# Kernel optimization log

Measured on AMD Instinct MI355X. Metric: run time of the kernel, lower is better.

Reference implementation:

```python
import jax, jax.numpy as jnp
import numpy as np

B, S, D, H, W = 8, 2048, 128, 8, 64
INT_HEADS = 8          # hardcoded in SpatioTemporalLayer1
EPS_COS = 1e-8
EPS_LN = 1e-5


def _mha(q_in, k_in, v_in, in_w, in_b, out_w, out_b, nh, mask=None):
    # q_in/k_in/v_in: (batch, len, d); torch nn.MultiheadAttention math (eval, no dropout)
    b, lq, d = q_in.shape
    hd = d // nh
    q = (q_in @ in_w[:d].T + in_b[:d]).reshape(b, lq, nh, hd)
    k = (k_in @ in_w[d:2 * d].T + in_b[d:2 * d]).reshape(b, k_in.shape[1], nh, hd)
    v = (v_in @ in_w[2 * d:].T + in_b[2 * d:]).reshape(b, v_in.shape[1], nh, hd)
    scores = jnp.einsum('bihd,bjhd->bhij', q, k) / jnp.sqrt(jnp.asarray(hd, q_in.dtype))
    if mask is not None:
        scores = scores + mask
    attn = jax.nn.softmax(scores, axis=-1)
    out = jnp.einsum('bhij,bjhd->bihd', attn, v).reshape(b, lq, d)
    return out @ out_w.T + out_b


def _layernorm(x, g, b):
    mu = x.mean(-1, keepdims=True)
    var = ((x - mu) ** 2).mean(-1, keepdims=True)
    return (x - mu) * jax.lax.rsqrt(var + EPS_LN) * g + b


def _cos_normalize(e):
    n = jnp.maximum(jnp.linalg.norm(e, axis=-1, keepdims=True), EPS_COS)
    return e / n


def _forward(x, spatial_info, temporal_info,
             lw_in_w, lw_in_b, lw_out_w, lw_out_b,
             spat_w, spat_b, temp_w, temp_b,
             int_in_w, int_in_b, int_out_w, int_out_b,
             ffn_w1, ffn_b1, ffn_w2, ffn_b2,
             ln1_g, ln1_b, ln2_g, ln2_b):
    b, s, d = x.shape
    # --- local window attention (S % W == 0 here, so no padding path) ---
    nw = s // W
    xw = x.reshape(b * nw, W, d)
    causal = jnp.triu(jnp.full((W, W), -jnp.inf, x.dtype), k=1)
    attn = _mha(xw, xw, xw, lw_in_w, lw_in_b, lw_out_w, lw_out_b, H, causal).reshape(b, s, d)
    x = _layernorm(attn + x, ln1_g, ln1_b)
    # --- FFN (torch nn.GELU default = exact erf) ---
    h = jax.nn.gelu(x @ ffn_w1.T + ffn_b1, approximate=False)
    x = _layernorm(h @ ffn_w2.T + ffn_b2 + x, ln2_g, ln2_b)
    # --- spatio-temporal interaction ---
    se = spatial_info @ spat_w.T + spat_b
    te = temporal_info @ temp_w.T + temp_b
    sn = _cos_normalize(se)
    tn = _cos_normalize(te)
    ss = jnp.einsum('bid,bjd->bij', sn, sn)   # (B,S,S) spatial cosine sim
    ts = jnp.einsum('bid,bjd->bij', tn, tn)   # (B,S,S) temporal cosine sim
    # interaction MHA is batch_first=False: it treats (B,S,D) as (len=B, batch=S, d).
    # Equivalent batch-first call on swapped axes (faithful to the torch source).
    inter = jnp.swapaxes(
        _mha(jnp.swapaxes(se, 0, 1), jnp.swapaxes(te, 0, 1), jnp.swapaxes(te, 0, 1),
             int_in_w, int_in_b, int_out_w, int_out_b, INT_HEADS), 0, 1)
    # similarity[b,i,j,d] = ss[b,i,j]*ts[b,i,j]*inter[b,i,d]; mean over j factorizes:
    sim = (ss * ts).mean(axis=2)              # (B,S)
    return x + sim[..., None] * inter


def setup_inputs() -> dict:
    key = jax.random.key(0)
    ks = jax.random.split(key, 24)
    sc = 0.02
    inp = {
        'x': jax.random.normal(ks[0], (B, S, D), jnp.float32),
        'spatial_info': jax.random.normal(ks[1], (B, S, D), jnp.float32),
        'temporal_info': jax.random.normal(ks[2], (B, S, D), jnp.float32),
        'lw_in_w': jax.random.normal(ks[3], (3 * D, D), jnp.float32) * sc,
        'lw_in_b': jnp.zeros((3 * D,), jnp.float32),
        'lw_out_w': jax.random.normal(ks[4], (D, D), jnp.float32) * sc,
        'lw_out_b': jnp.zeros((D,), jnp.float32),
        'spat_w': jax.random.normal(ks[5], (D, D), jnp.float32) * sc,
        'spat_b': jnp.zeros((D,), jnp.float32),
        'temp_w': jax.random.normal(ks[6], (D, D), jnp.float32) * sc,
        'temp_b': jnp.zeros((D,), jnp.float32),
        'int_in_w': jax.random.normal(ks[7], (3 * D, D), jnp.float32) * sc,
        'int_in_b': jnp.zeros((3 * D,), jnp.float32),
        'int_out_w': jax.random.normal(ks[8], (D, D), jnp.float32) * sc,
        'int_out_b': jnp.zeros((D,), jnp.float32),
        'ffn_w1': jax.random.normal(ks[9], (4 * D, D), jnp.float32) * sc,
        'ffn_b1': jnp.zeros((4 * D,), jnp.float32),
        'ffn_w2': jax.random.normal(ks[10], (D, 4 * D), jnp.float32) * sc,
        'ffn_b2': jnp.zeros((D,), jnp.float32),
        'ln1_g': jnp.ones((D,), jnp.float32),
        'ln1_b': jnp.zeros((D,), jnp.float32),
        'ln2_g': jnp.ones((D,), jnp.float32),
        'ln2_b': jnp.zeros((D,), jnp.float32),
    }
    return inp


def reference(x, spatial_info, temporal_info,
              lw_in_w, lw_in_b, lw_out_w, lw_out_b,
              spat_w, spat_b, temp_w, temp_b,
              int_in_w, int_in_b, int_out_w, int_out_b,
              ffn_w1, ffn_b1, ffn_w2, ffn_b2,
              ln1_g, ln1_b, ln2_g, ln2_b):
    return _forward(x, spatial_info, temporal_info,
                    lw_in_w, lw_in_b, lw_out_w, lw_out_b,
                    spat_w, spat_b, temp_w, temp_b,
                    int_in_w, int_in_b, int_out_w, int_out_b,
                    ffn_w1, ffn_b1, ffn_w2, ffn_b2,
                    ln1_g, ln1_b, ln2_g, ln2_b)
```

## Files before the change

kernel.cpp:

```cpp
#include <hip/hip_runtime.h>
#include <math.h>

#define BB 8
#define SS 2048
#define NTOK (BB * SS)

using bf16x8 = __attribute__((ext_vector_type(8))) short;
using f32x4  = __attribute__((ext_vector_type(4))) float;

__device__ __forceinline__ float gelu_tanh(float x) {
    float y = 0.7978845608f * (x + 0.044715f * x * x * x);
    float e = __expf(2.0f * y);
    float t = 1.0f - 2.0f / (e + 1.0f);
    return 0.5f * x * (1.0f + t);
}
__device__ __forceinline__ unsigned short f2b(float f) {
    unsigned int u = __float_as_uint(f);
    u += 0x7FFFu + ((u >> 16) & 1u);
    return (unsigned short)(u >> 16);
}
__device__ __forceinline__ float b2f(unsigned short u) {
    return __uint_as_float((unsigned int)u << 16);
}
__device__ __forceinline__ bf16x8 ldg_f32_b8(const float* p) {
    float4 f0 = *(const float4*)p, f1 = *(const float4*)(p + 4);
    union { ushort4 u[2]; bf16x8 v; } r;
    r.u[0] = (ushort4){f2b(f0.x), f2b(f0.y), f2b(f0.z), f2b(f0.w)};
    r.u[1] = (ushort4){f2b(f1.x), f2b(f1.y), f2b(f1.z), f2b(f1.w)};
    return r.v;
}

__global__ __launch_bounds__(256) void phase1(
    const float* __restrict__ x,
    const float* __restrict__ lw_in_w, const float* __restrict__ b_in,
    const float* __restrict__ lw_out_w, const float* __restrict__ b_out,
    const float* __restrict__ lng, const float* __restrict__ lnb,
    float* __restrict__ x1, unsigned short* __restrict__ x1b,
    const float* __restrict__ ffn_w1, const float* __restrict__ ffn_w2,
    unsigned short* __restrict__ Wb,
    const float* __restrict__ int_in_w, const float* __restrict__ int_out_w,
    unsigned short* __restrict__ Wib, unsigned short* __restrict__ Wiob,
    float* __restrict__ Mf,
    const float* __restrict__ spatial, const float* __restrict__ temporal,
    const float* __restrict__ spat_w, const float* __restrict__ temp_w,
    const float* __restrict__ bsp, const float* __restrict__ btp,
    unsigned short* __restrict__ snb, unsigned short* __restrict__ tnb,
    unsigned short* __restrict__ seb, unsigned short* __restrict__ teb)
{
    __shared__ unsigned short Qs[64 * 136];
    __shared__ unsigned short Ks[64 * 136];
    __shared__ unsigned short Vt[128 * 72];
    __shared__ unsigned short Pb[4][32 * 72];
    __shared__ float red[2][64][2];
    const int tid = threadIdx.x;
    const int wv = tid >> 6, lane = tid & 63, ln = lane & 15, q = lane >> 4;

    if (blockIdx.x >= 320) {
        const int idx2 = blockIdx.x - 320;
        const int y = idx2 >> 8;
        const int m0 = (idx2 & 255) * 64;
        const float* Af = y ? temporal : spatial;
        const float* Wf = y ? temp_w : spat_w;
        const float* bias = y ? btp : bsp;
        unsigned short* nb = y ? tnb : snb;
        unsigned short* raw = y ? teb : seb;
        const int wm = (wv >> 1) * 32, wn = (wv & 1) * 64;

        f32x4 acc[2][4] = {};
        #pragma unroll
        for (int kf = 0; kf < 4; ++kf) {
            bf16x8 a[2], b[4];
            #pragma unroll
            for (int fm = 0; fm < 2; ++fm)
                a[fm] = ldg_f32_b8(Af + (size_t)(m0 + wm + fm * 16 + ln) * 128 + kf * 32 + q * 8);
            #pragma unroll
            for (int fn = 0; fn < 4; ++fn)
                b[fn] = ldg_f32_b8(Wf + (size_t)(wn + fn * 16 + ln) * 128 + kf * 32 + q * 8);
            #pragma unroll
            for (int fm = 0; fm < 2; ++fm)
                #pragma unroll
                for (int fn = 0; fn < 4; ++fn)
                    acc[fm][fn] = __builtin_amdgcn_mfma_f32_16x16x32_bf16(a[fm], b[fn], acc[fm][fn], 0, 0, 0);
        }
        #pragma unroll
        for (int fm = 0; fm < 2; ++fm)
            #pragma unroll
            for (int r = 0; r < 4; ++r) {
                int rl = wm + fm * 16 + q * 4 + r;
                float s2 = 0.0f;
                #pragma unroll
                for (int fn = 0; fn < 4; ++fn) {
                    int col = wn + fn * 16 + ln;
                    float vv = acc[fm][fn][r] + bias[col];
                    acc[fm][fn][r] = vv;
                    s2 += vv * vv;
                }
                #pragma unroll
                for (int off = 1; off < 16; off <<= 1) s2 += __shfl_xor(s2, off, 64);
                if (ln == 0) red[0][rl][wv & 1] = s2;
            }
        __syncthreads();
        #pragma unroll
        for (int fm = 0; fm < 2; ++fm)
            #pragma unroll
            for (int r = 0; r < 4; ++r) {
                int rl = wm + fm * 16 + q * 4 + r;
                int row = m0 + rl;
                float inv = 1.0f / fmaxf(sqrtf(red[0][rl][0] + red[0][rl][1]), 1e-8f);
                #pragma unroll
                for (int fn = 0; fn < 4; ++fn) {
                    int col = wn + fn * 16 + ln;
                    float vv = acc[fm][fn][r];
                    nb[(size_t)row * 128 + col] = f2b(vv * inv);
                    raw[(size_t)row * 128 + col] = f2b(vv);
                }
            }
        return;
    }

    if (blockIdx.x >= 256) {
        int gt = (blockIdx.x - 256) * 256 + tid;
        #pragma unroll
        for (int s = 0; s < 3; ++s) {
            int v = gt + s * 16384;
            const float* src;
            unsigned short* dst;
            int off;
            if (v < 16384)      { src = ffn_w1;   dst = Wb;         off = v; }
            else if (v < 32768) { src = ffn_w2;   dst = Wb + 65536; off = v - 16384; }
            else if (v < 45056) { src = int_in_w; dst = Wib;        off = v - 32768; }
            else                { src = int_out_w; dst = Wiob;      off = v - 45056; }
            float4 f = *(const float4*)(src + (size_t)off * 4);
            *(ushort4*)(dst + (size_t)off * 4) =
                (ushort4){f2b(f.x), f2b(f.y), f2b(f.z), f2b(f.w)};
        }
        float4 z4 = (float4){0.f, 0.f, 0.f, 0.f};
        *(float4*)(Mf + (size_t)gt * 4) = z4;
        *(float4*)(Mf + (size_t)(gt + 16384) * 4) = z4;
        return;
    }

    const int m0 = blockIdx.x * 64;
    const int wm = (wv >> 1) * 32, wn = (wv & 1) * 64;

    bf16x8 afr[4][2];
    #pragma unroll
    for (int kf = 0; kf < 4; ++kf)
        #pragma unroll
        for (int fm = 0; fm < 2; ++fm)
            afr[kf][fm] = ldg_f32_b8(x + (size_t)(m0 + wm + fm * 16 + ln) * 128 + kf * 32 + q * 8);

    #pragma unroll
    for (int p = 0; p < 3; ++p) {
        f32x4 acc[2][4] = {};
        #pragma unroll
        for (int kf = 0; kf < 4; ++kf) {
            bf16x8 b[4];
            #pragma unroll
            for (int fn = 0; fn < 4; ++fn)
                b[fn] = ldg_f32_b8(lw_in_w + (size_t)(p * 128 + wn + fn * 16 + ln) * 128 + kf * 32 + q * 8);
            #pragma unroll
            for (int fm = 0; fm < 2; ++fm)
                #pragma unroll
                for (int fn = 0; fn < 4; ++fn)
                    acc[fm][fn] = __builtin_amdgcn_mfma_f32_16x16x32_bf16(afr[kf][fm], b[fn], acc[fm][fn], 0, 0, 0);
        }
        #pragma unroll
        for (int fm = 0; fm < 2; ++fm)
            #pragma unroll
            for (int r = 0; r < 4; ++r) {
                int rl = wm + fm * 16 + q * 4 + r;
                #pragma unroll
                for (int fn = 0; fn < 4; ++fn) {
                    int col = wn + fn * 16 + ln;
                    unsigned short v = f2b(acc[fm][fn][r] + b_in[p * 128 + col]);
                    if (p == 0)      Qs[rl * 136 + col] = v;
                    else if (p == 1) Ks[rl * 136 + col] = v;
                    else             Vt[col * 72 + rl] = v;
                }
            }
    }
    __syncthreads();

    {
        const int mh = wv >> 1, hq = wv & 1;
        unsigned short* P = &Pb[wv][0];
        #pragma unroll
        for (int hh = 0; hh < 4; ++hh) {
            const int h = hq * 4 + hh;
            f32x4 sacc[2][4] = {};
            bf16x8 az[2] = {}, bz[4] = {};
            if (q < 2) {
                #pragma unroll
                for (int fm = 0; fm < 2; ++fm)
                    az[fm] = *(const bf16x8*)&Qs[(mh * 32 + fm * 16 + ln) * 136 + h * 16 + q * 8];
                #pragma unroll
                for (int fn = 0; fn < 4; ++fn)
                    bz[fn] = *(const bf16x8*)&Ks[(fn * 16 + ln) * 136 + h * 16 + q * 8];
            }
            #pragma unroll
            for (int fm = 0; fm < 2; ++fm)
                #pragma unroll
                for (int fn = 0; fn < 4; ++fn)
                    sacc[fm][fn] = __builtin_amdgcn_mfma_f32_16x16x32_bf16(az[fm], bz[fn], sacc[fm][fn], 0, 0, 0);
            float invr[2][4];
            #pragma unroll
            for (int fm = 0; fm < 2; ++fm)
                #pragma unroll
                for (int r = 0; r < 4; ++r) {
                    int gi = mh * 32 + fm * 16 + q * 4 + r;
                    float mx = -1e30f;
                    #pragma unroll
                    for (int fn = 0; fn < 4; ++fn) {
                        int j = fn * 16 + ln;
                        float s = sacc[fm][fn][r] * 0.25f;
                        if (j > gi) s = -1e30f;
                        sacc[fm][fn][r] = s;
                        mx = fmaxf(mx, s);
                    }
                    #pragma unroll
                    for (int off = 1; off < 16; off <<= 1)
                        mx = fmaxf(mx, __shfl_xor(mx, off, 64));
                    float sum = 0.0f;
                    #pragma unroll
                    for (int fn = 0; fn < 4; ++fn) {
                        float p_ = __expf(sacc[fm][fn][r] - mx);
                        sacc[fm][fn][r] = p_;
                        sum += p_;
                    }
                    #pragma unroll
                    for (int off = 1; off < 16; off <<= 1)
                        sum += __shfl_xor(sum, off, 64);
                    invr[fm][r] = 1.0f / sum;
                    #pragma unroll
                    for (int fn = 0; fn < 4; ++fn)
                        P[(fm * 16 + q * 4 + r) * 72 + fn * 16 + ln] = f2b(sacc[fm][fn][r]);
                }
            f32x4 oacc[2] = {};
            #pragma unroll
            for (int kf2 = 0; kf2 < 2; ++kf2) {
                bf16x8 pa[2], vb;
                #pragma unroll
                for (int fm = 0; fm < 2; ++fm)
                    pa[fm] = *(const bf16x8*)&P[(fm * 16 + ln) * 72 + kf2 * 32 + q * 8];
                vb = *(const bf16x8*)&Vt[(h * 16 + ln) * 72 + kf2 * 32 + q * 8];
                #pragma unroll
                for (int fm = 0; fm < 2; ++fm)
                    oacc[fm] = __builtin_amdgcn_mfma_f32_16x16x32_bf16(pa[fm], vb, oacc[fm], 0, 0, 0);
            }
            #pragma unroll
            for (int fm = 0; fm < 2; ++fm)
                #pragma unroll
                for (int r = 0; r < 4; ++r)
                    Qs[(mh * 32 + fm * 16 + q * 4 + r) * 136 + h * 16 + ln] =
                        f2b(oacc[fm][r] * invr[fm][r]);
        }
    }
    __syncthreads();

    f32x4 acc[2][4] = {};
    #pragma unroll
    for (int kf = 0; kf < 4; ++kf) {
        bf16x8 a[2], b[4];
        #pragma unroll
        for (int fm = 0; fm < 2; ++fm)
            a[fm] = *(const bf16x8*)&Qs[(wm + fm * 16 + ln) * 136 + kf * 32 + q * 8];
        #pragma unroll
        for (int fn = 0; fn < 4; ++fn)
            b[fn] = ldg_f32_b8(lw_out_w + (size_t)(wn + fn * 16 + ln) * 128 + kf * 32 + q * 8);
        #pragma unroll
        for (int fm = 0; fm < 2; ++fm)
            #pragma unroll
            for (int fn = 0; fn < 4; ++fn)
                acc[fm][fn] = __builtin_amdgcn_mfma_f32_16x16x32_bf16(a[fm], b[fn], acc[fm][fn], 0, 0, 0);
    }
    #pragma unroll
    for (int fm = 0; fm < 2; ++fm)
        #pragma unroll
        for (int r = 0; r < 4; ++r) {
            int rl = wm + fm * 16 + q * 4 + r;
            int row = m0 + rl;
            float s1 = 0.0f, s2 = 0.0f;
            #pragma unroll
            for (int fn = 0; fn < 4; ++fn) {
                int col = wn + fn * 16 + ln;
                float vv = acc[fm][fn][r] + b_out[col] + x[(size_t)row * 128 + col];
                acc[fm][fn][r] = vv;
                s1 += vv; s2 += vv * vv;
            }
            #pragma unroll
            for (int off = 1; off < 16; off <<= 1) {
                s1 += __shfl_xor(s1, off, 64);
                s2 += __shfl_xor(s2, off, 64);
            }
            if (ln == 0) { red[0][rl][wv & 1] = s1; red[1][rl][wv & 1] = s2; }
        }
    __syncthreads();
    #pragma unroll
    for (int fm = 0; fm < 2; ++fm)
        #pragma unroll
        for (int r = 0; r < 4; ++r) {
            int rl = wm + fm * 16 + q * 4 + r;
            int row = m0 + rl;
            float mu = (red[0][rl][0] + red[0][rl][1]) * (1.0f / 128.0f);
            float var = (red[1][rl][0] + red[1][rl][1]) * (1.0f / 128.0f) - mu * mu;
            float rs = rsqrtf(var + 1e-5f);
            #pragma unroll
            for (int fn = 0; fn < 4; ++fn) {
                int col = wn + fn * 16 + ln;
                float o = (acc[fm][fn][r] - mu) * rs * lng[col] + lnb[col];
                x1[(size_t)row * 128 + col] = o;
                x1b[(size_t)row * 128 + col] = f2b(o);
            }
        }
}

__global__ __launch_bounds__(256) void phase2(
    const unsigned short* __restrict__ x1b, const float* __restrict__ x1,
    const unsigned short* __restrict__ Wb,
    const float* __restrict__ b1, const float* __restrict__ b2,
    const float* __restrict__ lng, const float* __restrict__ lnb,
    float* __restrict__ x2,
    const unsigned short* __restrict__ snb, const unsigned short* __restrict__ tnb,
    float* __restrict__ Mf)
{
    __shared__ __align__(16) char pool[36864];
    __shared__ float red[2][64][2];
    const int tid = threadIdx.x;
    const int wv = tid >> 6, lane = tid & 63, ln = lane & 15, q = lane >> 4;

    if (blockIdx.x < 256) {
        unsigned short* Xs = (unsigned short*)pool;
        unsigned short* Hs0 = (unsigned short*)(pool + 17408);
        unsigned short* Hs1 = (unsigned short*)(pool + 26624);
        const int t0 = blockIdx.x * 64;
        const int wm = (wv >> 1) * 32;
        const int wn1 = (wv & 1) * 32, wn2 = (wv & 1) * 64;
        const unsigned short* w1 = Wb;
        const unsigned short* w2 = Wb + 65536;

        const uint4* X4 = (const uint4*)(x1b + (size_t)t0 * 128);
        #pragma unroll
        for (int t = 0; t < 4; ++t) {
            int idx = tid + t * 256;
            int r = idx >> 4, c = idx & 15;
            *(uint4*)&Xs[r * 136 + c * 8] = X4[r * 16 + c];
        }
        __syncthreads();

        f32x4 acc2[2][4] = {};
        for (int ch = 0; ch < 8; ++ch) {
            const int hc0 = ch * 64;
            unsigned short* Hb = (ch & 1) ? Hs1 : Hs0;
            f32x4 acc1[2][2] = {};
            #pragma unroll
            for (int kf = 0; kf < 4; ++kf) {
                bf16x8 a[2], b[2];
                #pragma unroll
                for (int fm = 0; fm < 2; ++fm)
                    a[fm] = *(const bf16x8*)&Xs[(wm + fm * 16 + ln) * 136 + kf * 32 + q * 8];
                #pragma unroll
                for (int fn = 0; fn < 2; ++fn)
                    b[fn] = *(const bf16x8*)&w1[(size_t)(hc0 + wn1 + fn * 16 + ln) * 128 + kf * 32 + q * 8];
                #pragma unroll
                for (int fm = 0; fm < 2; ++fm)
                    #pragma unroll
                    for (int fn = 0; fn < 2; ++fn)
                        acc1[fm][fn] = __builtin_amdgcn_mfma_f32_16x16x32_bf16(a[fm], b[fn], acc1[fm][fn], 0, 0, 0);
            }
            #pragma unroll
            for (int fm = 0; fm < 2; ++fm)
                #pragma unroll
                for (int fn = 0; fn < 2; ++fn)
                    #pragma unroll
                    for (int r = 0; r < 4; ++r) {
                        int rl = wm + fm * 16 + q * 4 + r;
                        int col = wn1 + fn * 16 + ln;
                        Hb[rl * 72 + col] = f2b(gelu_tanh(acc1[fm][fn][r] + b1[hc0 + col]));
                    }
            __syncthreads();
            #pragma unroll
            for (int kf2 = 0; kf2 < 2; ++kf2) {
                bf16x8 a[2], b[4];
                #pragma unroll
                for (int fm = 0; fm < 2; ++fm)
                    a[fm] = *(const bf16x8*)&Hb[(wm + fm * 16 + ln) * 72 + kf2 * 32 + q * 8];
                #pragma unroll
                for (int fn = 0; fn < 4; ++fn)
                    b[fn] = *(const bf16x8*)&w2[(size_t)(wn2 + fn * 16 + ln) * 512 + hc0 + kf2 * 32 + q * 8];
                #pragma unroll
                for (int fm = 0; fm < 2; ++fm)
                    #pragma unroll
                    for (int fn = 0; fn < 4; ++fn)
                        acc2[fm][fn] = __builtin_amdgcn_mfma_f32_16x16x32_bf16(a[fm], b[fn], acc2[fm][fn], 0, 0, 0);
            }
        }
        #pragma unroll
        for (int fm = 0; fm < 2; ++fm)
            #pragma unroll
            for (int r = 0; r < 4; ++r) {
                int rl = wm + fm * 16 + q * 4 + r;
                int row = t0 + rl;
                float s1 = 0.0f, s2 = 0.0f;
                #pragma unroll
                for (int fn = 0; fn < 4; ++fn) {
                    int col = wn2 + fn * 16 + ln;
                    float vv = acc2[fm][fn][r] + b2[col] + x1[(size_t)row * 128 + col];
                    acc2[fm][fn][r] = vv;
                    s1 += vv; s2 += vv * vv;
                }
                #pragma unroll
                for (int off = 1; off < 16; off <<= 1) {
                    s1 += __shfl_xor(s1, off, 64);
                    s2 += __shfl_xor(s2, off, 64);
                }
                if (ln == 0) { red[0][rl][wv & 1] = s1; red[1][rl][wv & 1] = s2; }
            }
        __syncthreads();
        #pragma unroll
        for (int fm = 0; fm < 2; ++fm)
            #pragma unroll
            for (int r = 0; r < 4; ++r) {
                int rl = wm + fm * 16 + q * 4 + r;
                int row = t0 + rl;
                float mu = (red[0][rl][0] + red[0][rl][1]) * (1.0f / 128.0f);
                float var = (red[1][rl][0] + red[1][rl][1]) * (1.0f / 128.0f) - mu * mu;
                float rs = rsqrtf(var + 1e-5f);
                #pragma unroll
                for (int fn = 0; fn < 4; ++fn) {
                    int col = wn2 + fn * 16 + ln;
                    x2[(size_t)row * 128 + col] = (acc2[fm][fn][r] - mu) * rs * lng[col] + lnb[col];
                }
            }
        return;
    }

    {
        unsigned short* Sst = (unsigned short*)pool;
        unsigned short* Tst = (unsigned short*)(pool + 17408);
        const int idx2 = blockIdx.x - 256;
        const int d0 = (idx2 & 1) * 64, e0 = ((idx2 >> 1) & 1) * 64;
        const int z = idx2 >> 2;
        const int b = z >> 4, chunk = z & 15;
        const size_t rowb = (size_t)(b * SS + chunk * 128);

        #pragma unroll
        for (int it = 0; it < 4; ++it) {
            int j = (tid & 31) + it * 32;
            int c8 = (tid >> 5) * 8;
            uint4 sv = *(const uint4*)&snb[(rowb + j) * 128 + d0 + c8];
            uint4 tv = *(const uint4*)&tnb[(rowb + j) * 128 + e0 + c8];
            const unsigned short* sp = (const unsigned short*)&sv;
            const unsigned short* tp = (const unsigned short*)&tv;
            #pragma unroll
            for (int c = 0; c < 8; ++c) {
                Sst[(c8 + c) * 136 + j] = sp[c];
                Tst[(c8 + c) * 136 + j] = tp[c];
            }
        }
        __syncthreads();

        const int wm = (wv >> 1) * 32, wn = (wv & 1) * 32;
        f32x4 acc[2][2] = {};
        #pragma unroll
        for (int kf = 0; kf < 4; ++kf) {
            bf16x8 a[2], bb[2];
            #pragma unroll
            for (int fm = 0; fm < 2; ++fm)
                a[fm] = *(const bf16x8*)&Tst[(wm + fm * 16 + ln) * 136 + kf * 32 + q * 8];
            #pragma unroll
            for (int fn = 0; fn < 2; ++fn)
                bb[fn] = *(const bf16x8*)&Sst[(wn + fn * 16 + ln) * 136 + kf * 32 + q * 8];
            #pragma unroll
            for (int fm = 0; fm < 2; ++fm)
                #pragma unroll
                for (int fn = 0; fn < 2; ++fn)
                    acc[fm][fn] = __builtin_amdgcn_mfma_f32_16x16x32_bf16(a[fm], bb[fn], acc[fm][fn], 0, 0, 0);
        }
        float* pp = Mf + (size_t)b * 16384;
        #pragma unroll
        for (int fm = 0; fm < 2; ++fm)
            #pragma unroll
            for (int r = 0; r < 4; ++r) {
                int ee = e0 + wm + fm * 16 + q * 4 + r;
                #pragma unroll
                for (int fn = 0; fn < 2; ++fn) {
                    int dd = d0 + wn + fn * 16 + ln;
                    unsafeAtomicAdd(&pp[(size_t)ee * 128 + dd], acc[fm][fn][r]);
                }
            }
    }
}

__global__ __launch_bounds__(256) void simgemm_kernel(
    const unsigned short* __restrict__ snb, const unsigned short* __restrict__ tnb,
    const float* __restrict__ Mf, float* __restrict__ sim)
{
    __shared__ float red[64][2];
    const int tid = threadIdx.x, m0 = blockIdx.x * 64, b = m0 >> 11;
    const int wv = tid >> 6, lane = tid & 63, ln = lane & 15, q = lane >> 4;
    const int wm = (wv >> 1) * 32, wn = (wv & 1) * 64;

    f32x4 acc[2][4] = {};
    #pragma unroll
    for (int kf = 0; kf < 4; ++kf) {
        bf16x8 a[2], bb[4];
        #pragma unroll
        for (int fm = 0; fm < 2; ++fm)
            a[fm] = *(const bf16x8*)&snb[(size_t)(m0 + wm + fm * 16 + ln) * 128 + kf * 32 + q * 8];
        #pragma unroll
        for (int fn = 0; fn < 4; ++fn)
            bb[fn] = ldg_f32_b8(Mf + (size_t)b * 16384 + (size_t)(wn + fn * 16 + ln) * 128 + kf * 32 + q * 8);
        #pragma unroll
        for (int fm = 0; fm < 2; ++fm)
            #pragma unroll
            for (int fn = 0; fn < 4; ++fn)
                acc[fm][fn] = __builtin_amdgcn_mfma_f32_16x16x32_bf16(a[fm], bb[fn], acc[fm][fn], 0, 0, 0);
    }
    #pragma unroll
    for (int fm = 0; fm < 2; ++fm)
        #pragma unroll
        for (int r = 0; r < 4; ++r) {
            int rl = wm + fm * 16 + q * 4 + r;
            int row = m0 + rl;
            float s = 0.0f;
            #pragma unroll
            for (int fn = 0; fn < 4; ++fn) {
                int col = wn + fn * 16 + ln;
                s += acc[fm][fn][r] * b2f(tnb[(size_t)row * 128 + col]);
            }
            #pragma unroll
            for (int off = 1; off < 16; off <<= 1) s += __shfl_xor(s, off, 64);
            if (ln == 0) red[rl][wv & 1] = s;
        }
    __syncthreads();
    if (tid < 64) sim[m0 + tid] = (red[tid][0] + red[tid][1]) * (1.0f / (float)SS);
}

__global__ __launch_bounds__(256) void inter_block(
    const unsigned short* __restrict__ seb, const unsigned short* __restrict__ teb,
    const unsigned short* __restrict__ Wib,
    const float* __restrict__ b_int,
    const unsigned short* __restrict__ Wiob,
    const float* __restrict__ b_io,
    const float* __restrict__ sim, const float* __restrict__ x2,
    float* __restrict__ out)
{
    __shared__ unsigned short Qs[64 * 136];
    __shared__ unsigned short KVs[64 * 256];
    const int tid = threadIdx.x, s0 = blockIdx.x * 8;
    const int wv = tid >> 6, lane = tid & 63, ln = lane & 15, q = lane >> 4;
    const int wm = (wv >> 1) * 32, wn = (wv & 1) * 64;

    bf16x8 afr[4][2];
    #pragma unroll
    for (int kf = 0; kf < 4; ++kf)
        #pragma unroll
        for (int fm = 0; fm < 2; ++fm) {
            int rl = wm + fm * 16 + ln;
            size_t g = (size_t)(rl >> 3) * 2048 + s0 + (rl & 7);
            afr[kf][fm] = *(const bf16x8*)&seb[g * 128 + kf * 32 + q * 8];
        }

    #pragma unroll
    for (int p = 0; p < 3; ++p) {
        if (p == 1) {
            #pragma unroll
            for (int kf = 0; kf < 4; ++kf)
                #pragma unroll
                for (int fm = 0; fm < 2; ++fm) {
                    int rl = wm + fm * 16 + ln;
                    size_t g = (size_t)(rl >> 3) * 2048 + s0 + (rl & 7);
                    afr[kf][fm] = *(const bf16x8*)&teb[g * 128 + kf * 32 + q * 8];
                }
        }
        f32x4 acc[2][4] = {};
        #pragma unroll
        for (int kf = 0; kf < 4; ++kf) {
            bf16x8 b[4];
            #pragma unroll
            for (int fn = 0; fn < 4; ++fn)
                b[fn] = *(const bf16x8*)&Wib[(size_t)(p * 128 + wn + fn * 16 + ln) * 128 + kf * 32 + q * 8];
            #pragma unroll
            for (int fm = 0; fm < 2; ++fm)
                #pragma unroll
                for (int fn = 0; fn < 4; ++fn)
                    acc[fm][fn] = __builtin_amdgcn_mfma_f32_16x16x32_bf16(afr[kf][fm], b[fn], acc[fm][fn], 0, 0, 0);
        }
        #pragma unroll
        for (int fm = 0; fm < 2; ++fm)
            #pragma unroll
            for (int r = 0; r < 4; ++r) {
                int rl = wm + fm * 16 + q * 4 + r;
                #pragma unroll
                for (int fn = 0; fn < 4; ++fn) {
                    int col = wn + fn * 16 + ln;
                    unsigned short v = f2b(acc[fm][fn][r] + b_int[p * 128 + col]);
                    if (p == 0) Qs[rl * 136 + col] = v;
                    else        KVs[rl * 256 + (p - 1) * 128 + col] = v;
                }
            }
        __syncthreads();
    }

    #pragma unroll
    for (int tt = 0; tt < 2; ++tt) {
        int task = tid + tt * 256;
        int ss = task >> 6, h = (task >> 3) & 7, i = task & 7;
        int rq = i * 8 + ss;
        float qr[16];
        {
            uint4 q0 = *(const uint4*)&Qs[rq * 136 + h * 16];
            uint4 q1 = *(const uint4*)&Qs[rq * 136 + h * 16 + 8];
            const unsigned short* p0 = (const unsigned short*)&q0;
            const unsigned short* p1 = (const unsigned short*)&q1;
            #pragma unroll
            for (int c = 0; c < 8; ++c) { qr[c] = b2f(p0[c]); qr[8 + c] = b2f(p1[c]); }
        }
        float sc[8];
        #pragma unroll
        for (int j = 0; j < 8; ++j) {
            uint4 k0 = *(const uint4*)&KVs[(j * 8 + ss) * 256 + h * 16];
            uint4 k1 = *(const uint4*)&KVs[(j * 8 + ss) * 256 + h * 16 + 8];
            const unsigned short* kp0 = (const unsigned short*)&k0;
            const unsigned short* kp1 = (const unsigned short*)&k1;
            float s = 0.0f;
            #pragma unroll
            for (int c = 0; c < 8; ++c) {
                s = fmaf(qr[c], b2f(kp0[c]), s);
                s = fmaf(qr[8 + c], b2f(kp1[c]), s);
            }
            sc[j] = s * 0.25f;
        }
        float mx = -1e30f;
        #pragma unroll
        for (int j = 0; j < 8; ++j) mx = fmaxf(mx, sc[j]);
        float pe[8], se = 0.0f;
        #pragma unroll
        for (int j = 0; j < 8; ++j) { pe[j] = __expf(sc[j] - mx); se += pe[j]; }
        float inv = 1.0f / se;
        float o[16] = {};
        #pragma unroll
        for (int j = 0; j < 8; ++j) {
            uint4 v0 = *(const uint4*)&KVs[(j * 8 + ss) * 256 + 128 + h * 16];
            uint4 v1 = *(const uint4*)&KVs[(j * 8 + ss) * 256 + 128 + h * 16 + 8];
            const unsigned short* vp0 = (const unsigned short*)&v0;
            const unsigned short* vp1 = (const unsigned short*)&v1;
            #pragma unroll
            for (int c = 0; c < 8; ++c) {
                o[c]     += pe[j] * b2f(vp0[c]);
                o[8 + c] += pe[j] * b2f(vp1[c]);
            }
        }
        ushort4 w0 = (ushort4){f2b(o[0]*inv),  f2b(o[1]*inv),  f2b(o[2]*inv),  f2b(o[3]*inv)};
        ushort4 w1 = (ushort4){f2b(o[4]*inv),  f2b(o[5]*inv),  f2b(o[6]*inv),  f2b(o[7]*inv)};
        ushort4 w2 = (ushort4){f2b(o[8]*inv),  f2b(o[9]*inv),  f2b(o[10]*inv), f2b(o[11]*inv)};
        ushort4 w3 = (ushort4){f2b(o[12]*inv), f2b(o[13]*inv), f2b(o[14]*inv), f2b(o[15]*inv)};
        *(ushort4*)&Qs[rq * 136 + h * 16]      = w0;
        *(ushort4*)&Qs[rq * 136 + h * 16 + 4]  = w1;
        *(ushort4*)&Qs[rq * 136 + h * 16 + 8]  = w2;
        *(ushort4*)&Qs[rq * 136 + h * 16 + 12] = w3;
    }
    __syncthreads();

    f32x4 acc[2][4] = {};
    #pragma unroll
    for (int kf = 0; kf < 4; ++kf) {
        bf16x8 a[2], b[4];
        #pragma unroll
        for (int fm = 0; fm < 2; ++fm)
            a[fm] = *(const bf16x8*)&Qs[(wm + fm * 16 + ln) * 136 + kf * 32 + q * 8];
        #pragma unroll
        for (int fn = 0; fn < 4; ++fn)
            b[fn] = *(const bf16x8*)&Wiob[(size_t)(wn + fn * 16 + ln) * 128 + kf * 32 + q * 8];
        #pragma unroll
        for (int fm = 0; fm < 2; ++fm)
            #pragma unroll
            for (int fn = 0; fn < 4; ++fn)
                acc[fm][fn] = __builtin_amdgcn_mfma_f32_16x16x32_bf16(a[fm], b[fn], acc[fm][fn], 0, 0, 0);
    }
    #pragma unroll
    for (int fm = 0; fm < 2; ++fm)
        #pragma unroll
        for (int r = 0; r < 4; ++r) {
            int rl = wm + fm * 16 + q * 4 + r;
            size_t g = (size_t)(rl >> 3) * 2048 + s0 + (rl & 7);
            float sc = sim[g];
            #pragma unroll
            for (int fn = 0; fn < 4; ++fn) {
                int col = wn + fn * 16 + ln;
                out[g * 128 + col] = (acc[fm][fn][r] + b_io[col]) * sc + x2[g * 128 + col];
            }
        }
}

extern "C" void kernel_launch(void* const* d_in, const int* in_sizes, int n_in,
                              void* d_out, int out_size, void* d_ws, size_t ws_size,
                              hipStream_t stream)
{
    const float* x        = (const float*)d_in[0];
    const float* spatial  = (const float*)d_in[1];
    const float* temporal = (const float*)d_in[2];
    const float* lw_in_w  = (const float*)d_in[3];
    const float* lw_in_b  = (const float*)d_in[4];
    const float* lw_out_w = (const float*)d_in[5];
    const float* lw_out_b = (const float*)d_in[6];
    const float* spat_w   = (const float*)d_in[7];
    const float* spat_b   = (const float*)d_in[8];
    const float* temp_w   = (const float*)d_in[9];
    const float* temp_b   = (const float*)d_in[10];
    const float* int_in_w = (const float*)d_in[11];
    const float* int_in_b = (const float*)d_in[12];
    const float* int_out_w= (const float*)d_in[13];
    const float* int_out_b= (const float*)d_in[14];
    const float* ffn_b1   = (const float*)d_in[16];
    const float* ffn_b2   = (const float*)d_in[18];
    const float* ln1_g    = (const float*)d_in[19];
    const float* ln1_b    = (const float*)d_in[20];
    const float* ln2_g    = (const float*)d_in[21];
    const float* ln2_b    = (const float*)d_in[22];
    float* out = (float*)d_out;

    char* base = (char*)d_ws;
    float*          x1   = (float*)(base + 0);
    unsigned short* x1b  = (unsigned short*)(base + 8388608);
    float*          x2   = (float*)(base + 12582912);
    unsigned short* snb  = (unsigned short*)(base + 20971520);
    unsigned short* tnb  = (unsigned short*)(base + 25165824);
    unsigned short* seb  = (unsigned short*)(base + 29360128);
    unsigned short* teb  = (unsigned short*)(base + 33554432);
    unsigned short* Wb   = (unsigned short*)(base + 37748736);
    unsigned short* Wib  = (unsigned short*)(base + 38010880);
    unsigned short* Wiob = (unsigned short*)(base + 38109184);
    float*          Mf   = (float*)(base + 38141952);
    float*          simb = (float*)(base + 38666240);

    phase1<<<832, 256, 0, stream>>>(
        x, lw_in_w, lw_in_b, lw_out_w, lw_out_b, ln1_g, ln1_b, x1, x1b,
        (const float*)d_in[15], (const float*)d_in[17], Wb,
        int_in_w, int_out_w, Wib, Wiob, Mf,
        spatial, temporal, spat_w, temp_w, spat_b, temp_b,
        snb, tnb, seb, teb);
    phase2<<<768, 256, 0, stream>>>(
        x1b, x1, Wb, ffn_b1, ffn_b2, ln2_g, ln2_b, x2, snb, tnb, Mf);
    simgemm_kernel<<<256, 256, 0, stream>>>(snb, tnb, Mf, simb);
    inter_block<<<256, 256, 0, stream>>>(
        seb, teb, Wib, int_in_b, Wiob, int_out_b, simb, x2, out);
}
```

Measured before the change: 219.1 us.

## Rebalance phase1 to 512-thread blocks and give each FFN wave full rows

Phase1 now runs 512 threads per block across 512 blocks. In the attention blocks each of 8 waves handles 16 query rows instead of 32. The weight conversion, Mf zeroing and spatial/temporal projection blocks are merged, each projection block covering 128 rows. In phase2's FFN each wave owns 16 full token rows across all 128 output columns. This removes the shared X staging, the per-chunk __syncthreads, and the cross-wave LayerNorm reduction in favour of shuffles only. The goals are fewer barriers, less LDS traffic and better occupancy. The cost is higher register pressure (8 accumulators) and each wave reading all of w2 on its own.

```diff
diff --git a/kernel.cpp b/kernel.cpp
--- a/kernel.cpp
+++ b/kernel.cpp
@@ -30,7 +30,7 @@
     return r.v;
 }
 
-__global__ __launch_bounds__(256) void phase1(
+__global__ __launch_bounds__(512) void phase1(
     const float* __restrict__ x,
     const float* __restrict__ lw_in_w, const float* __restrict__ b_in,
     const float* __restrict__ lw_out_w, const float* __restrict__ b_out,
@@ -50,21 +50,37 @@
     __shared__ unsigned short Qs[64 * 136];
     __shared__ unsigned short Ks[64 * 136];
     __shared__ unsigned short Vt[128 * 72];
-    __shared__ unsigned short Pb[4][32 * 72];
-    __shared__ float red[2][64][2];
+    __shared__ unsigned short Pb[8][16 * 72];
+    __shared__ float red[2][128][2];
     const int tid = threadIdx.x;
     const int wv = tid >> 6, lane = tid & 63, ln = lane & 15, q = lane >> 4;
 
-    if (blockIdx.x >= 320) {
-        const int idx2 = blockIdx.x - 320;
-        const int y = idx2 >> 8;
-        const int m0 = (idx2 & 255) * 64;
+    if (blockIdx.x >= 256) {
+        const int sidx = blockIdx.x - 256;
+        if (sidx < 96) {
+            int v = sidx * 512 + tid;
+            const float* src; unsigned short* dst; int off;
+            if (v < 16384)      { src = ffn_w1;    dst = Wb;         off = v; }
+            else if (v < 32768) { src = ffn_w2;    dst = Wb + 65536; off = v - 16384; }
+            else if (v < 45056) { src = int_in_w;  dst = Wib;        off = v - 32768; }
+            else                { src = int_out_w; dst = Wiob;       off = v - 45056; }
+            float4 f = *(const float4*)(src + (size_t)off * 4);
+            *(ushort4*)(dst + (size_t)off * 4) =
+                (ushort4){f2b(f.x), f2b(f.y), f2b(f.z), f2b(f.w)};
+        } else if (sidx < 160) {
+            int gt = (sidx - 96) * 512 + tid;
+            *(float4*)(Mf + (size_t)gt * 4) = (float4){0.f, 0.f, 0.f, 0.f};
+        }
+        const int y = sidx >> 7;
+        const int m0 = (sidx & 127) * 128;
         const float* Af = y ? temporal : spatial;
         const float* Wf = y ? temp_w : spat_w;
         const float* bias = y ? btp : bsp;
         unsigned short* nb = y ? tnb : snb;
         unsigned short* raw = y ? teb : seb;
-        const int wm = (wv >> 1) * 32, wn = (wv & 1) * 64;
+        const int sub = wv >> 2, w4 = wv & 3;
+        const int wm = (w4 >> 1) * 32, wn = (w4 & 1) * 64;
+        const int r0 = m0 + sub * 64;
 
         f32x4 acc[2][4] = {};
         #pragma unroll
@@ -72,7 +88,7 @@
             bf16x8 a[2], b[4];
             #pragma unroll
             for (int fm = 0; fm < 2; ++fm)
-                a[fm] = ldg_f32_b8(Af + (size_t)(m0 + wm + fm * 16 + ln) * 128 + kf * 32 + q * 8);
+                a[fm] = ldg_f32_b8(Af + (size_t)(r0 + wm + fm * 16 + ln) * 128 + kf * 32 + q * 8);
             #pragma unroll
             for (int fn = 0; fn < 4; ++fn)
                 b[fn] = ldg_f32_b8(Wf + (size_t)(wn + fn * 16 + ln) * 128 + kf * 32 + q * 8);
@@ -86,7 +102,7 @@
         for (int fm = 0; fm < 2; ++fm)
             #pragma unroll
             for (int r = 0; r < 4; ++r) {
-                int rl = wm + fm * 16 + q * 4 + r;
+                int rlg = sub * 64 + wm + fm * 16 + q * 4 + r;
                 float s2 = 0.0f;
                 #pragma unroll
                 for (int fn = 0; fn < 4; ++fn) {
@@ -97,16 +113,16 @@
                 }
                 #pragma unroll
                 for (int off = 1; off < 16; off <<= 1) s2 += __shfl_xor(s2, off, 64);
-                if (ln == 0) red[0][rl][wv & 1] = s2;
+                if (ln == 0) red[0][rlg][w4 & 1] = s2;
             }
         __syncthreads();
         #pragma unroll
         for (int fm = 0; fm < 2; ++fm)
             #pragma unroll
             for (int r = 0; r < 4; ++r) {
-                int rl = wm + fm * 16 + q * 4 + r;
-                int row = m0 + rl;
-                float inv = 1.0f / fmaxf(sqrtf(red[0][rl][0] + red[0][rl][1]), 1e-8f);
+                int rlg = sub * 64 + wm + fm * 16 + q * 4 + r;
+                int row = m0 + rlg;
+                float inv = 1.0f / fmaxf(sqrtf(red[0][rlg][0] + red[0][rlg][1]), 1e-8f);
                 #pragma unroll
                 for (int fn = 0; fn < 4; ++fn) {
                     int col = wn + fn * 16 + ln;
@@ -118,41 +134,17 @@
         return;
     }
 
-    if (blockIdx.x >= 256) {
-        int gt = (blockIdx.x - 256) * 256 + tid;
-        #pragma unroll
-        for (int s = 0; s < 3; ++s) {
-            int v = gt + s * 16384;
-            const float* src;
-            unsigned short* dst;
-            int off;
-            if (v < 16384)      { src = ffn_w1;   dst = Wb;         off = v; }
-            else if (v < 32768) { src = ffn_w2;   dst = Wb + 65536; off = v - 16384; }
-            else if (v < 45056) { src = int_in_w; dst = Wib;        off = v - 32768; }
-            else                { src = int_out_w; dst = Wiob;      off = v - 45056; }
-            float4 f = *(const float4*)(src + (size_t)off * 4);
-            *(ushort4*)(dst + (size_t)off * 4) =
-                (ushort4){f2b(f.x), f2b(f.y), f2b(f.z), f2b(f.w)};
-        }
-        float4 z4 = (float4){0.f, 0.f, 0.f, 0.f};
-        *(float4*)(Mf + (size_t)gt * 4) = z4;
-        *(float4*)(Mf + (size_t)(gt + 16384) * 4) = z4;
-        return;
-    }
-
     const int m0 = blockIdx.x * 64;
-    const int wm = (wv >> 1) * 32, wn = (wv & 1) * 64;
-
-    bf16x8 afr[4][2];
+    const int wm4 = (wv >> 1) * 16, wn = (wv & 1) * 64;
+
+    bf16x8 afr[4];
     #pragma unroll
     for (int kf = 0; kf < 4; ++kf)
-        #pragma unroll
-        for (int fm = 0; fm < 2; ++fm)
-            afr[kf][fm] = ldg_f32_b8(x + (size_t)(m0 + wm + fm * 16 + ln) * 128 + kf * 32 + q * 8);
+        afr[kf] = ldg_f32_b8(x + (size_t)(m0 + wm4 + ln) * 128 + kf * 32 + q * 8);
 
     #pragma unroll
     for (int p = 0; p < 3; ++p) {
-        f32x4 acc[2][4] = {};
+        f32x4 acc[4] = {};
         #pragma unroll
         for (int kf = 0; kf < 4; ++kf) {
             bf16x8 b[4];
@@ -160,159 +152,133 @@
             for (int fn = 0; fn < 4; ++fn)
                 b[fn] = ldg_f32_b8(lw_in_w + (size_t)(p * 128 + wn + fn * 16 + ln) * 128 + kf * 32 + q * 8);
             #pragma unroll
-            for (int fm = 0; fm < 2; ++fm)
-                #pragma unroll
-                for (int fn = 0; fn < 4; ++fn)
-                    acc[fm][fn] = __builtin_amdgcn_mfma_f32_16x16x32_bf16(afr[kf][fm], b[fn], acc[fm][fn], 0, 0, 0);
-        }
-        #pragma unroll
-        for (int fm = 0; fm < 2; ++fm)
-            #pragma unroll
-            for (int r = 0; r < 4; ++r) {
-                int rl = wm + fm * 16 + q * 4 + r;
-                #pragma unroll
-                for (int fn = 0; fn < 4; ++fn) {
-                    int col = wn + fn * 16 + ln;
-                    unsigned short v = f2b(acc[fm][fn][r] + b_in[p * 128 + col]);
-                    if (p == 0)      Qs[rl * 136 + col] = v;
-                    else if (p == 1) Ks[rl * 136 + col] = v;
-                    else             Vt[col * 72 + rl] = v;
-                }
-            }
+            for (int fn = 0; fn < 4; ++fn)
+                acc[fn] = __builtin_amdgcn_mfma_f32_16x16x32_bf16(afr[kf], b[fn], acc[fn], 0, 0, 0);
+        }
+        #pragma unroll
+        for (int r = 0; r < 4; ++r) {
+            int rl = wm4 + q * 4 + r;
+            #pragma unroll
+            for (int fn = 0; fn < 4; ++fn) {
+                int col = wn + fn * 16 + ln;
+                unsigned short v = f2b(acc[fn][r] + b_in[p * 128 + col]);
+                if (p == 0)      Qs[rl * 136 + col] = v;
+                else if (p == 1) Ks[rl * 136 + col] = v;
+                else             Vt[col * 72 + rl] = v;
+            }
+        }
     }
     __syncthreads();
 
     {
-        const int mh = wv >> 1, hq = wv & 1;
+        const int mh3 = wv >> 1, hq = wv & 1;
         unsigned short* P = &Pb[wv][0];
         #pragma unroll
         for (int hh = 0; hh < 4; ++hh) {
             const int h = hq * 4 + hh;
-            f32x4 sacc[2][4] = {};
-            bf16x8 az[2] = {}, bz[4] = {};
+            f32x4 sacc[4] = {};
+            bf16x8 az = {}, bz[4] = {};
             if (q < 2) {
-                #pragma unroll
-                for (int fm = 0; fm < 2; ++fm)
-                    az[fm] = *(const bf16x8*)&Qs[(mh * 32 + fm * 16 + ln) * 136 + h * 16 + q * 8];
+                az = *(const bf16x8*)&Qs[(mh3 * 16 + ln) * 136 + h * 16 + q * 8];
                 #pragma unroll
                 for (int fn = 0; fn < 4; ++fn)
                     bz[fn] = *(const bf16x8*)&Ks[(fn * 16 + ln) * 136 + h * 16 + q * 8];
             }
             #pragma unroll
-            for (int fm = 0; fm < 2; ++fm)
+            for (int fn = 0; fn < 4; ++fn)
+                sacc[fn] = __builtin_amdgcn_mfma_f32_16x16x32_bf16(az, bz[fn], sacc[fn], 0, 0, 0);
+            float invr[4];
+            #pragma unroll
+            for (int r = 0; r < 4; ++r) {
+                int gi = mh3 * 16 + q * 4 + r;
+                float mx = -1e30f;
+                #pragma unroll
+                for (int fn = 0; fn < 4; ++fn) {
+                    int j = fn * 16 + ln;
+                    float s = sacc[fn][r] * 0.25f;
+                    if (j > gi) s = -1e30f;
+                    sacc[fn][r] = s;
+                    mx = fmaxf(mx, s);
+                }
+                #pragma unroll
+                for (int off = 1; off < 16; off <<= 1)
+                    mx = fmaxf(mx, __shfl_xor(mx, off, 64));
+                float sum = 0.0f;
+                #pragma unroll
+                for (int fn = 0; fn < 4; ++fn) {
+                    float p_ = __expf(sacc[fn][r] - mx);
+                    sacc[fn][r] = p_;
+                    sum += p_;
+                }
+                #pragma unroll
+                for (int off = 1; off < 16; off <<= 1)
+                    sum += __shfl_xor(sum, off, 64);
+                invr[r] = 1.0f / sum;
                 #pragma unroll
                 for (int fn = 0; fn < 4; ++fn)
-                    sacc[fm][fn] = __builtin_amdgcn_mfma_f32_16x16x32_bf16(az[fm], bz[fn], sacc[fm][fn], 0, 0, 0);
-            float invr[2][4];
-            #pragma unroll
-            for (int fm = 0; fm < 2; ++fm)
-                #pragma unroll
-                for (int r = 0; r < 4; ++r) {
-                    int gi = mh * 32 + fm * 16 + q * 4 + r;
-                    float mx = -1e30f;
-                    #pragma unroll
-                    for (int fn = 0; fn < 4; ++fn) {
-                        int j = fn * 16 + ln;
-                        float s = sacc[fm][fn][r] * 0.25f;
-                        if (j > gi) s = -1e30f;
-                        sacc[fm][fn][r] = s;
-                        mx = fmaxf(mx, s);
-                    }
-                    #pragma unroll
-                    for (int off = 1; off < 16; off <<= 1)
-                        mx = fmaxf(mx, __shfl_xor(mx, off, 64));
-                    float sum = 0.0f;
-                    #pragma unroll
-                    for (int fn = 0; fn < 4; ++fn) {
-                        float p_ = __expf(sacc[fm][fn][r] - mx);
-                        sacc[fm][fn][r] = p_;
-                        sum += p_;
-                    }
-                    #pragma unroll
-                    for (int off = 1; off < 16; off <<= 1)
-                        sum += __shfl_xor(sum, off, 64);
-                    invr[fm][r] = 1.0f / sum;
-                    #pragma unroll
-                    for (int fn = 0; fn < 4; ++fn)
-                        P[(fm * 16 + q * 4 + r) * 72 + fn * 16 + ln] = f2b(sacc[fm][fn][r]);
-                }
-            f32x4 oacc[2] = {};
+                    P[(q * 4 + r) * 72 + fn * 16 + ln] = f2b(sacc[fn][r]);
+            }
+            f32x4 oacc = {};
             #pragma unroll
             for (int kf2 = 0; kf2 < 2; ++kf2) {
-                bf16x8 pa[2], vb;
-                #pragma unroll
-                for (int fm = 0; fm < 2; ++fm)
-                    pa[fm] = *(const bf16x8*)&P[(fm * 16 + ln) * 72 + kf2 * 32 + q * 8];
-                vb = *(const bf16x8*)&Vt[(h * 16 + ln) * 72 + kf2 * 32 + q * 8];
-                #pragma unroll
-                for (int fm = 0; fm < 2; ++fm)
-                    oacc[fm] = __builtin_amdgcn_mfma_f32_16x16x32_bf16(pa[fm], vb, oacc[fm], 0, 0, 0);
-            }
-            #pragma unroll
-            for (int fm = 0; fm < 2; ++fm)
-                #pragma unroll
-                for (int r = 0; r < 4; ++r)
-                    Qs[(mh * 32 + fm * 16 + q * 4 + r) * 136 + h * 16 + ln] =
-                        f2b(oacc[fm][r] * invr[fm][r]);
+                bf16x8 pa = *(const bf16x8*)&P[ln * 72 + kf2 * 32 + q * 8];
+                bf16x8 vb = *(const bf16x8*)&Vt[(h * 16 + ln) * 72 + kf2 * 32 + q * 8];
+                oacc = __builtin_amdgcn_mfma_f32_16x16x32_bf16(pa, vb, oacc, 0, 0, 0);
+            }
+            #pragma unroll
+            for (int r = 0; r < 4; ++r)
+                Qs[(mh3 * 16 + q * 4 + r) * 136 + h * 16 + ln] = f2b(oacc[r] * invr[r]);
         }
     }
     __syncthreads();
 
-    f32x4 acc[2][4] = {};
+    f32x4 acc[4] = {};
     #pragma unroll
     for (int kf = 0; kf < 4; ++kf) {
-        bf16x8 a[2], b[4];
-        #pragma unroll
-        for (int fm = 0; fm < 2; ++fm)
-            a[fm] = *(const bf16x8*)&Qs[(wm + fm * 16 + ln) * 136 + kf * 32 + q * 8];
+        bf16x8 a = *(const bf16x8*)&Qs[(wm4 + ln) * 136 + kf * 32 + q * 8];
+        bf16x8 b[4];
         #pragma unroll
         for (int fn = 0; fn < 4; ++fn)
             b[fn] = ldg_f32_b8(lw_out_w + (size_t)(wn + fn * 16 + ln) * 128 + kf * 32 + q * 8);
         #pragma unroll
-        for (int fm = 0; fm < 2; ++fm)
-            #pragma unroll
-            for (int fn = 0; fn < 4; ++fn)
-                acc[fm][fn] = __builtin_amdgcn_mfma_f32_16x16x32_bf16(a[fm], b[fn], acc[fm][fn], 0, 0, 0);
-    }
-    #pragma unroll
-    for (int fm = 0; fm < 2; ++fm)
-        #pragma unroll
-        for (int r = 0; r < 4; ++r) {
-            int rl = wm + fm * 16 + q * 4 + r;
-            int row = m0 + rl;
-            float s1 = 0.0f, s2 = 0.0f;
-            #pragma unroll
-            for (int fn = 0; fn < 4; ++fn) {
-                int col = wn + fn * 16 + ln;
-                float vv = acc[fm][fn][r] + b_out[col] + x[(size_t)row * 128 + col];
-                acc[fm][fn][r] = vv;
-                s1 += vv; s2 += vv * vv;
-            }
-            #pragma unroll
-            for (int off = 1; off < 16; off <<= 1) {
-                s1 += __shfl_xor(s1, off, 64);
-                s2 += __shfl_xor(s2, off, 64);
-            }
-            if (ln == 0) { red[0][rl][wv & 1] = s1; red[1][rl][wv & 1] = s2; }
-        }
+        for (int fn = 0; fn < 4; ++fn)
+            acc[fn] = __builtin_amdgcn_mfma_f32_16x16x32_bf16(a, b[fn], acc[fn], 0, 0, 0);
+    }
+    #pragma unroll
+    for (int r = 0; r < 4; ++r) {
+        int rl = wm4 + q * 4 + r;
+        int row = m0 + rl;
+        float s1 = 0.0f, s2 = 0.0f;
+        #pragma unroll
+        for (int fn = 0; fn < 4; ++fn) {
+            int col = wn + fn * 16 + ln;
+            float vv = acc[fn][r] + b_out[col] + x[(size_t)row * 128 + col];
+            acc[fn][r] = vv;
+            s1 += vv; s2 += vv * vv;
+        }
+        #pragma unroll
+        for (int off = 1; off < 16; off <<= 1) {
+            s1 += __shfl_xor(s1, off, 64);
+            s2 += __shfl_xor(s2, off, 64);
+        }
+        if (ln == 0) { red[0][rl][wv & 1] = s1; red[1][rl][wv & 1] = s2; }
+    }
     __syncthreads();
     #pragma unroll
-    for (int fm = 0; fm < 2; ++fm)
-        #pragma unroll
-        for (int r = 0; r < 4; ++r) {
-            int rl = wm + fm * 16 + q * 4 + r;
-            int row = m0 + rl;
-            float mu = (red[0][rl][0] + red[0][rl][1]) * (1.0f / 128.0f);
-            float var = (red[1][rl][0] + red[1][rl][1]) * (1.0f / 128.0f) - mu * mu;
-            float rs = rsqrtf(var + 1e-5f);
-            #pragma unroll
-            for (int fn = 0; fn < 4; ++fn) {
-                int col = wn + fn * 16 + ln;
-                float o = (acc[fm][fn][r] - mu) * rs * lng[col] + lnb[col];
-                x1[(size_t)row * 128 + col] = o;
-                x1b[(size_t)row * 128 + col] = f2b(o);
-            }
-        }
+    for (int r = 0; r < 4; ++r) {
+        int rl = wm4 + q * 4 + r;
+        int row = m0 + rl;
+        float mu = (red[0][rl][0] + red[0][rl][1]) * (1.0f / 128.0f);
+        float var = (red[1][rl][0] + red[1][rl][1]) * (1.0f / 128.0f) - mu * mu;
+        float rs = rsqrtf(var + 1e-5f);
+        #pragma unroll
+        for (int fn = 0; fn < 4; ++fn) {
+            int col = wn + fn * 16 + ln;
+            float o = (acc[fn][r] - mu) * rs * lng[col] + lnb[col];
+            x1[(size_t)row * 128 + col] = o;
+            x1b[(size_t)row * 128 + col] = f2b(o);
+        }
+    }
 }
 
 __global__ __launch_bounds__(256) void phase2(
@@ -324,114 +290,79 @@
     const unsigned short* __restrict__ snb, const unsigned short* __restrict__ tnb,
     float* __restrict__ Mf)
 {
-    __shared__ __align__(16) char pool[36864];
-    __shared__ float red[2][64][2];
+    __shared__ __align__(16) char pool[34816];
     const int tid = threadIdx.x;
     const int wv = tid >> 6, lane = tid & 63, ln = lane & 15, q = lane >> 4;
 
     if (blockIdx.x < 256) {
-        unsigned short* Xs = (unsigned short*)pool;
-        unsigned short* Hs0 = (unsigned short*)(pool + 17408);
-        unsigned short* Hs1 = (unsigned short*)(pool + 26624);
+        unsigned short* Hw = (unsigned short*)pool + wv * 1152;
         const int t0 = blockIdx.x * 64;
-        const int wm = (wv >> 1) * 32;
-        const int wn1 = (wv & 1) * 32, wn2 = (wv & 1) * 64;
+        const int wm1 = wv * 16;
         const unsigned short* w1 = Wb;
         const unsigned short* w2 = Wb + 65536;
 
-        const uint4* X4 = (const uint4*)(x1b + (size_t)t0 * 128);
-        #pragma unroll
-        for (int t = 0; t < 4; ++t) {
-            int idx = tid + t * 256;
-            int r = idx >> 4, c = idx & 15;
-            *(uint4*)&Xs[r * 136 + c * 8] = X4[r * 16 + c];
-        }
-        __syncthreads();
-
-        f32x4 acc2[2][4] = {};
+        bf16x8 afr[4];
+        #pragma unroll
+        for (int kf = 0; kf < 4; ++kf)
+            afr[kf] = *(const bf16x8*)&x1b[(size_t)(t0 + wm1 + ln) * 128 + kf * 32 + q * 8];
+
+        f32x4 acc2[8] = {};
         for (int ch = 0; ch < 8; ++ch) {
             const int hc0 = ch * 64;
-            unsigned short* Hb = (ch & 1) ? Hs1 : Hs0;
-            f32x4 acc1[2][2] = {};
+            f32x4 acc1[4] = {};
             #pragma unroll
             for (int kf = 0; kf < 4; ++kf) {
-                bf16x8 a[2], b[2];
-                #pragma unroll
-                for (int fm = 0; fm < 2; ++fm)
-                    a[fm] = *(const bf16x8*)&Xs[(wm + fm * 16 + ln) * 136 + kf * 32 + q * 8];
-                #pragma unroll
-                for (int fn = 0; fn < 2; ++fn)
-                    b[fn] = *(const bf16x8*)&w1[(size_t)(hc0 + wn1 + fn * 16 + ln) * 128 + kf * 32 + q * 8];
-                #pragma unroll
-                for (int fm = 0; fm < 2; ++fm)
-                    #pragma unroll
-                    for (int fn = 0; fn < 2; ++fn)
-                        acc1[fm][fn] = __builtin_amdgcn_mfma_f32_16x16x32_bf16(a[fm], b[fn], acc1[fm][fn], 0, 0, 0);
-            }
-            #pragma unroll
-            for (int fm = 0; fm < 2; ++fm)
-                #pragma unroll
-                for (int fn = 0; fn < 2; ++fn)
-                    #pragma unroll
-                    for (int r = 0; r < 4; ++r) {
-                        int rl = wm + fm * 16 + q * 4 + r;
-                        int col = wn1 + fn * 16 + ln;
-                        Hb[rl * 72 + col] = f2b(gelu_tanh(acc1[fm][fn][r] + b1[hc0 + col]));
-                    }
-            __syncthreads();
+                bf16x8 b[4];
+                #pragma unroll
+                for (int fn = 0; fn < 4; ++fn)
+                    b[fn] = *(const bf16x8*)&w1[(size_t)(hc0 + fn * 16 + ln) * 128 + kf * 32 + q * 8];
+                #pragma unroll
+                for (int fn = 0; fn < 4; ++fn)
+                    acc1[fn] = __builtin_amdgcn_mfma_f32_16x16x32_bf16(afr[kf], b[fn], acc1[fn], 0, 0, 0);
+            }
+            #pragma unroll
+            for (int fn = 0; fn < 4; ++fn)
+                #pragma unroll
+                for (int r = 0; r < 4; ++r)
+                    Hw[(q * 4 + r) * 72 + fn * 16 + ln] =
+                        f2b(gelu_tanh(acc1[fn][r] + b1[hc0 + fn * 16 + ln]));
             #pragma unroll
             for (int kf2 = 0; kf2 < 2; ++kf2) {
-                bf16x8 a[2], b[4];
-                #pragma unroll
-                for (int fm = 0; fm < 2; ++fm)
-                    a[fm] = *(const bf16x8*)&Hb[(wm + fm * 16 + ln) * 72 + kf2 * 32 + q * 8];
-                #pragma unroll
-                for (int fn = 0; fn < 4; ++fn)
-                    b[fn] = *(const bf16x8*)&w2[(size_t)(wn2 + fn * 16 + ln) * 512 + hc0 + kf2 * 32 + q * 8];
-                #pragma unroll
-                for (int fm = 0; fm < 2; ++fm)
-                    #pragma unroll
-                    for (int fn = 0; fn < 4; ++fn)
-                        acc2[fm][fn] = __builtin_amdgcn_mfma_f32_16x16x32_bf16(a[fm], b[fn], acc2[fm][fn], 0, 0, 0);
-            }
-        }
-        #pragma unroll
-        for (int fm = 0; fm < 2; ++fm)
-            #pragma unroll
-            for (int r = 0; r < 4; ++r) {
-                int rl = wm + fm * 16 + q * 4 + r;
-                int row = t0 + rl;
-                float s1 = 0.0f, s2 = 0.0f;
-                #pragma unroll
-                for (int fn = 0; fn < 4; ++fn) {
-                    int col = wn2 + fn * 16 + ln;
-                    float vv = acc2[fm][fn][r] + b2[col] + x1[(size_t)row * 128 + col];
-                    acc2[fm][fn][r] = vv;
-                    s1 += vv; s2 += vv * vv;
-                }
-                #pragma unroll
-                for (int off = 1; off < 16; off <<= 1) {
-                    s1 += __shfl_xor(s1, off, 64);
-                    s2 += __shfl_xor(s2, off, 64);
-                }
-                if (ln == 0) { red[0][rl][wv & 1] = s1; red[1][rl][wv & 1] = s2; }
-            }
-        __syncthreads();
-        #pragma unroll
-        for (int fm = 0; fm < 2; ++fm)
-            #pragma unroll
-            for (int r = 0; r < 4; ++r) {
-                int rl = wm + fm * 16 + q * 4 + r;
-                int row = t0 + rl;
-                float mu = (red[0][rl][0] + red[0][rl][1]) * (1.0f / 128.0f);
-                float var = (red[1][rl][0] + red[1][rl][1]) * (1.0f / 128.0f) - mu * mu;
-                float rs = rsqrtf(var + 1e-5f);
-                #pragma unroll
-                for (int fn = 0; fn < 4; ++fn) {
-                    int col = wn2 + fn * 16 + ln;
-                    x2[(size_t)row * 128 + col] = (acc2[fm][fn][r] - mu) * rs * lng[col] + lnb[col];
-                }
-            }
+                bf16x8 a = *(const bf16x8*)&Hw[ln * 72 + kf2 * 32 + q * 8];
+                bf16x8 b8[8];
+                #pragma unroll
+                for (int fn = 0; fn < 8; ++fn)
+                    b8[fn] = *(const bf16x8*)&w2[(size_t)(fn * 16 + ln) * 512 + hc0 + kf2 * 32 + q * 8];
+                #pragma unroll
+                for (int fn = 0; fn < 8; ++fn)
+                    acc2[fn] = __builtin_amdgcn_mfma_f32_16x16x32_bf16(a, b8[fn], acc2[fn], 0, 0, 0);
+            }
+        }
+        #pragma unroll
+        for (int r = 0; r < 4; ++r) {
+            int row = t0 + wm1 + q * 4 + r;
+            float s1 = 0.0f, s2 = 0.0f;
+            #pragma unroll
+            for (int fn = 0; fn < 8; ++fn) {
+                int col = fn * 16 + ln;
+                float vv = acc2[fn][r] + b2[col] + x1[(size_t)row * 128 + col];
+                acc2[fn][r] = vv;
+                s1 += vv; s2 += vv * vv;
+            }
+            #pragma unroll
+            for (int off = 1; off < 16; off <<= 1) {
+                s1 += __shfl_xor(s1, off, 64);
+                s2 += __shfl_xor(s2, off, 64);
+            }
+            float mu = s1 * (1.0f / 128.0f);
+            float var = s2 * (1.0f / 128.0f) - mu * mu;
+            float rs = rsqrtf(var + 1e-5f);
+            #pragma unroll
+            for (int fn = 0; fn < 8; ++fn) {
+                int col = fn * 16 + ln;
+                x2[(size_t)row * 128 + col] = (acc2[fn][r] - mu) * rs * lng[col] + lnb[col];
+            }
+        }
         return;
     }
 
@@ -735,7 +666,7 @@
     float*          Mf   = (float*)(base + 38141952);
     float*          simb = (float*)(base + 38666240);
 
-    phase1<<<832, 256, 0, stream>>>(
+    phase1<<<512, 512, 0, stream>>>(
         x, lw_in_w, lw_in_b, lw_out_w, lw_out_b, ln1_g, ln1_b, x1, x1b,
         (const float*)d_in[15], (const float*)d_in[17], Wb,
         int_in_w, int_out_w, Wib, Wiob, Mf,
```

Result: slower. 235.3 us (+7.4%).
